# Performance work log

Measured on AMD Instinct MI355X. Metric: run time of the kernel, lower is better.

Reference implementation:

```python
import jax, jax.numpy as jnp
import numpy as np

NUM_CIRCLES = 7
B, D_IN, D_HID, D_OUT = 4096, 2048, 3584, 2048  # D_HID % 7 == 0 (7 * 512)


def setup_inputs() -> dict:
    key = jax.random.key(0)
    k1, k2, k3, k4 = jax.random.split(key, 4)
    x = jax.random.normal(k1, (B, D_IN), dtype=jnp.float32)
    # FlowerOfLife: 7 bias-free Linear(D_IN -> D_HID//7) weights, stacked [7, D_HID//7, D_IN]
    W_flower = jax.random.normal(k2, (NUM_CIRCLES, D_HID // NUM_CIRCLES, D_IN), dtype=jnp.float32) / np.sqrt(D_IN).astype(np.float32)
    # Merkaba: two bias-free Linear(D_HID -> D_OUT)
    W_male = jax.random.normal(k3, (D_OUT, D_HID), dtype=jnp.float32) / np.sqrt(D_HID).astype(np.float32)
    W_female = jax.random.normal(k4, (D_OUT, D_HID), dtype=jnp.float32) / np.sqrt(D_HID).astype(np.float32)
    return {"x": x, "W_flower": W_flower, "W_male": W_male, "W_female": W_female}


def reference(x, W_flower, W_male, W_female):
    # --- VesicaPiscisOperation: sacred overlap with the batch-rolled neighbor ---
    x2 = jnp.roll(x, 1, axis=0)
    dist = jnp.linalg.norm(x - x2, axis=1, keepdims=True)          # [B, 1]
    overlap = jax.nn.relu(1.0 - jnp.abs(dist - 1.0))               # [B, 1]
    x_overlap = x * (1.0 + overlap)                                # per-row scaling

    # --- FlowerOfLifeProjection: 7 parallel projections, phase-shift first 2 dims ---
    circ = jnp.einsum('bd,cod->bco', x_overlap, W_flower)          # [B, 7, D_HID//7]
    phases = 2.0 * jnp.pi * jnp.arange(NUM_CIRCLES, dtype=jnp.float32) / NUM_CIRCLES
    phase_shift = jnp.stack([jnp.cos(phases), jnp.sin(phases)], axis=-1)  # [7, 2]
    circ = circ.at[:, :, :2].multiply(phase_shift[None, :, :])
    x_expanded = circ.reshape(x.shape[0], -1)                      # [B, D_HID]

    # --- MerkabaRotation: counter-rotating transforms + sigmoid phase lock ---
    male = x_expanded @ W_male.T                                   # [B, D_OUT]
    female = x_expanded[:, ::-1] @ W_female.T                      # flip(-1) then Linear
    phase_lock = jax.nn.sigmoid(jnp.sum(male * female, axis=-1, keepdims=True))
    return phase_lock * male + (1.0 - phase_lock) * female
```

## Files before the change

### kernel.cpp

```cpp
#include <hip/hip_runtime.h>
#include <hip/hip_bf16.h>
#include <math.h>

#define B_DIM 4096
#define D_IN  2048
#define D_HID 3584
#define D_OUT 2048

typedef __bf16 bf16;
typedef float  floatx4 __attribute__((ext_vector_type(4)));
typedef bf16   bf16x8  __attribute__((ext_vector_type(8)));
typedef bf16   bf16x4  __attribute__((ext_vector_type(4)));

typedef __attribute__((address_space(1))) const void* gptr1;
typedef __attribute__((address_space(3))) void*       lptr3;

__device__ __forceinline__ void load_lds16(const void* g, void* l) {
    __builtin_amdgcn_global_load_lds((gptr1)g, (lptr3)l, 16, 0, 0);
}

struct HL { bf16 h, l; };
__device__ __forceinline__ HL split2(float v) {
    HL r;
    r.h = (bf16)v;
    r.l = (bf16)(v - (float)r.h);
    return r;
}

__device__ __forceinline__ void xcd_tile(int& n0, int& m0) {
    const int d  = (int)(blockIdx.x + gridDim.x * blockIdx.y);
    const int r  = d >> 3;
    const int nx = ((d & 7) << 1) | (r & 1);
    const int my = r >> 1;
    n0 = nx * 128;
    m0 = my * 128;
}

__global__ __launch_bounds__(256) void vesica_kernel(const float* __restrict__ x,
                                                     bf16* __restrict__ xh,
                                                     bf16* __restrict__ xl) {
    const int b  = blockIdx.x;
    const int bp = (b == 0) ? (B_DIM - 1) : (b - 1);
    const int t  = threadIdx.x;

    const floatx4* xr = (const floatx4*)(x + (size_t)b  * D_IN);
    const floatx4* pr = (const floatx4*)(x + (size_t)bp * D_IN);
    const floatx4 v0 = xr[t * 2], v1 = xr[t * 2 + 1];
    const floatx4 p0 = pr[t * 2], p1 = pr[t * 2 + 1];

    float s = 0.f;
#pragma unroll
    for (int j = 0; j < 4; ++j) {
        const float d0 = v0[j] - p0[j], d1 = v1[j] - p1[j];
        s += d0 * d0 + d1 * d1;
    }
#pragma unroll
    for (int off = 32; off > 0; off >>= 1) s += __shfl_down(s, off, 64);

    __shared__ float red[4];
    const int wave = t >> 6, lane = t & 63;
    if (lane == 0) red[wave] = s;
    __syncthreads();
    const float dist = sqrtf(red[0] + red[1] + red[2] + red[3]);
    const float sc   = 1.f + fmaxf(0.f, 1.f - fabsf(dist - 1.f));

    bf16x8 h, l;
#pragma unroll
    for (int j = 0; j < 4; ++j) {
        const HL a  = split2(v0[j] * sc);
        const HL b2 = split2(v1[j] * sc);
        h[j] = a.h;      l[j] = a.l;
        h[4 + j] = b2.h; l[4 + j] = b2.l;
    }
    ((bf16x8*)(xh + (size_t)b * D_IN))[t] = h;
    ((bf16x8*)(xl + (size_t)b * D_IN))[t] = l;
}

__global__ __launch_bounds__(256) void wcat_kernel(const float* __restrict__ Wm,
                                                   const float* __restrict__ Wfe,
                                                   bf16* __restrict__ wh,
                                                   bf16* __restrict__ wl) {
    const int i = blockIdx.x * 256 + threadIdx.x;
    const int o = i / 448;
    const int g = i - o * 448;
    bf16x8 h, l;
    if (o < 2048) {
        const float* src = Wm + (size_t)o * 3584 + (size_t)g * 8;
        const floatx4 a = ((const floatx4*)src)[0];
        const floatx4 b = ((const floatx4*)src)[1];
#pragma unroll
        for (int j = 0; j < 4; ++j) {
            const HL u = split2(a[j]);
            const HL v = split2(b[j]);
            h[j] = u.h;     l[j] = u.l;
            h[4 + j] = v.h; l[4 + j] = v.l;
        }
    } else {
        const float* src = Wfe + (size_t)(o - 2048) * 3584 + (size_t)(447 - g) * 8;
        const floatx4 a = ((const floatx4*)src)[0];
        const floatx4 b = ((const floatx4*)src)[1];
#pragma unroll
        for (int j = 0; j < 4; ++j) {
            const HL u = split2(b[3 - j]);
            const HL v = split2(a[3 - j]);
            h[j] = u.h;     l[j] = u.l;
            h[4 + j] = v.h; l[4 + j] = v.l;
        }
    }
    ((bf16x8*)wh)[i] = h;
    ((bf16x8*)wl)[i] = l;
}

__global__ __launch_bounds__(256) void tsplit_kernel(const float* __restrict__ w,
                                                     bf16* __restrict__ th,
                                                     bf16* __restrict__ tl) {
    __shared__ float tile[64][65];
    const int d0 = blockIdx.x * 64;
    const int h0 = blockIdx.y * 64;
    const int t  = threadIdx.x;
    const int r  = t >> 4;
    const int cg = (t & 15) << 2;

#pragma unroll
    for (int i = 0; i < 4; ++i) {
        const int hr = r + i * 16;
        const floatx4 v = *(const floatx4*)&w[(size_t)(h0 + hr) * 2048 + d0 + cg];
        tile[hr][cg]     = v[0];
        tile[hr][cg + 1] = v[1];
        tile[hr][cg + 2] = v[2];
        tile[hr][cg + 3] = v[3];
    }
    __syncthreads();

    float pm[4];
#pragma unroll
    for (int j = 0; j < 4; ++j) {
        const int h  = h0 + cg + j;
        const int hm = h & 511;
        float p = 1.f;
        if (hm < 2) {
            const float ph = 0.8975979010256552f * (float)(h >> 9);
            p = (hm == 0) ? cosf(ph) : sinf(ph);
        }
        pm[j] = p;
    }

#pragma unroll
    for (int i = 0; i < 4; ++i) {
        const int dr = r + i * 16;
        bf16x4 hh, ll;
#pragma unroll
        for (int j = 0; j < 4; ++j) {
            const HL u = split2(tile[cg + j][dr] * pm[j]);
            hh[j] = u.h;
            ll[j] = u.l;
        }
        const size_t o = (size_t)(d0 + dr) * 3584 + h0 + cg;
        *(bf16x4*)&th[o] = hh;
        *(bf16x4*)&tl[o] = ll;
    }
}

__global__ __launch_bounds__(256, 2) void gemm3_single(const bf16* __restrict__ Ah,
                                                       const bf16* __restrict__ Al,
                                                       const bf16* __restrict__ Bh,
                                                       const bf16* __restrict__ Bl,
                                                       bf16* __restrict__ C0,
                                                       bf16* __restrict__ C1,
                                                       int M, int N, int K) {
    __shared__ bf16 sAh[128 * 64], sAl[128 * 64];
    __shared__ bf16 sBh[128 * 64], sBl[128 * 64];

    const int tid  = threadIdx.x;
    const int wave = tid >> 6;
    const int lane = tid & 63;
    int n0, m0;
    xcd_tile(n0, m0);
    const int wm   = wave & 1;
    const int wn   = wave >> 1;

    floatx4 acc[4][4];
#pragma unroll
    for (int i = 0; i < 4; ++i)
#pragma unroll
        for (int j = 0; j < 4; ++j) acc[i][j] = (floatx4){0.f, 0.f, 0.f, 0.f};

    const int lr  = lane & 15;
    const int cc8 = (lane >> 4) << 3;
    const int sw  = lr & 7;

    for (int kt = 0; kt < K; kt += 64) {
#pragma unroll
        for (int i = 0; i < 4; ++i) {
            const int q = ((i * 4 + wave) << 6) + lane;
            const int r = q >> 3;
            const int c = (q & 7) ^ (r & 7);
            const int e = q << 3;
            const size_t ga = (size_t)(m0 + r) * K + kt + c * 8;
            const size_t gb = (size_t)(n0 + r) * K + kt + c * 8;
            load_lds16(&Ah[ga], &sAh[e]);
            load_lds16(&Al[ga], &sAl[e]);
            load_lds16(&Bh[gb], &sBh[e]);
            load_lds16(&Bl[gb], &sBl[e]);
        }
        __syncthreads();

#pragma unroll
        for (int ks = 0; ks < 2; ++ks) {
            const int cb = (ks << 2) + (cc8 >> 3);
            const int co = (cb ^ sw) << 3;
            bf16x8 ah[4], al[4], bh[4], bl[4];
#pragma unroll
            for (int mi = 0; mi < 4; ++mi) {
                const int off = ((wm * 64 + mi * 16 + lr) << 6) + co;
                ah[mi] = *(const bf16x8*)&sAh[off];
                al[mi] = *(const bf16x8*)&sAl[off];
            }
#pragma unroll
            for (int ni = 0; ni < 4; ++ni) {
                const int off = ((wn * 64 + ni * 16 + lr) << 6) + co;
                bh[ni] = *(const bf16x8*)&sBh[off];
                bl[ni] = *(const bf16x8*)&sBl[off];
            }

#pragma unroll
            for (int mi = 0; mi < 4; ++mi)
#pragma unroll
                for (int ni = 0; ni < 4; ++ni) {
                    acc[mi][ni] = __builtin_amdgcn_mfma_f32_16x16x32_bf16(
                        ah[mi], bh[ni], acc[mi][ni], 0, 0, 0);
                    acc[mi][ni] = __builtin_amdgcn_mfma_f32_16x16x32_bf16(
                        al[mi], bh[ni], acc[mi][ni], 0, 0, 0);
                    acc[mi][ni] = __builtin_amdgcn_mfma_f32_16x16x32_bf16(
                        ah[mi], bl[ni], acc[mi][ni], 0, 0, 0);
                }
        }
        __syncthreads();
    }

    const int rq = (lane >> 4) << 2;
    const int cl = lane & 15;
#pragma unroll
    for (int mi = 0; mi < 4; ++mi) {
#pragma unroll
        for (int ni = 0; ni < 4; ++ni) {
            const int col = n0 + wn * 64 + ni * 16 + cl;
#pragma unroll
            for (int r = 0; r < 4; ++r) {
                const int row = m0 + wm * 64 + mi * 16 + rq + r;
                const size_t idx = (size_t)row * N + col;
                const HL u = split2(acc[mi][ni][r]);
                C0[idx] = u.h;
                C1[idx] = u.l;
            }
        }
    }
}

__global__ __launch_bounds__(256, 2) void gemm3_dual(const bf16* __restrict__ Ah,
                                                     const bf16* __restrict__ Al,
                                                     const bf16* __restrict__ Bmh,
                                                     const bf16* __restrict__ Bml,
                                                     const bf16* __restrict__ Bfh,
                                                     const bf16* __restrict__ Bfl,
                                                     float* __restrict__ Cm,
                                                     float* __restrict__ Cf,
                                                     int M, int N, int K) {
    __shared__ bf16 sAh[4096], sAl[4096];
    __shared__ bf16 sMh[4096], sMl[4096];
    __shared__ bf16 sFh[4096], sFl[4096];

    const int tid  = threadIdx.x;
    const int wave = tid >> 6;
    const int lane = tid & 63;
    int n0, m0;
    xcd_tile(n0, m0);
    const int wm   = wave & 1;
    const int wn   = wave >> 1;

    floatx4 am[4][4], af[4][4];
#pragma unroll
    for (int i = 0; i < 4; ++i)
#pragma unroll
        for (int j = 0; j < 4; ++j) {
            am[i][j] = (floatx4){0.f, 0.f, 0.f, 0.f};
            af[i][j] = (floatx4){0.f, 0.f, 0.f, 0.f};
        }

    const int lr  = lane & 15;
    const int cc8 = (lane >> 4) << 3;
    const int cq  = cc8 >> 3;
    const int hsw = lr >> 1;

    for (int kt = 0; kt < K; kt += 32) {
#pragma unroll
        for (int i = 0; i < 2; ++i) {
            const int q = ((i * 4 + wave) << 6) + lane;
            const int p = q ^ ((q >> 3) & 7);
            const int r = p >> 2, c = p & 3;
            const int e = q << 3;
            const size_t ga = (size_t)(m0 + r) * K + kt + c * 8;
            const size_t gb = (size_t)(n0 + r) * K + kt + c * 8;
            load_lds16(&Ah[ga],  &sAh[e]);
            load_lds16(&Al[ga],  &sAl[e]);
            load_lds16(&Bmh[gb], &sMh[e]);
            load_lds16(&Bml[gb], &sMl[e]);
            load_lds16(&Bfh[gb], &sFh[e]);
            load_lds16(&Bfl[gb], &sFl[e]);
        }
        __syncthreads();

        bf16x8 ah[4], al[4];
#pragma unroll
        for (int mi = 0; mi < 4; ++mi) {
            const int ql  = ((wm * 64 + mi * 16 + lr) << 2) + cq;
            const int off = (ql ^ hsw) << 3;
            ah[mi] = *(const bf16x8*)&sAh[off];
            al[mi] = *(const bf16x8*)&sAl[off];
        }
#pragma unroll
        for (int ni = 0; ni < 4; ++ni) {
            const int ql  = ((wn * 64 + ni * 16 + lr) << 2) + cq;
            const int off = (ql ^ hsw) << 3;
            const bf16x8 mh = *(const bf16x8*)&sMh[off];
            const bf16x8 ml = *(const bf16x8*)&sMl[off];
            const bf16x8 fh = *(const bf16x8*)&sFh[off];
            const bf16x8 fl = *(const bf16x8*)&sFl[off];
#pragma unroll
            for (int mi = 0; mi < 4; ++mi) {
                am[mi][ni] = __builtin_amdgcn_mfma_f32_16x16x32_bf16(
                    ah[mi], mh, am[mi][ni], 0, 0, 0);
                am[mi][ni] = __builtin_amdgcn_mfma_f32_16x16x32_bf16(
                    al[mi], mh, am[mi][ni], 0, 0, 0);
                am[mi][ni] = __builtin_amdgcn_mfma_f32_16x16x32_bf16(
                    ah[mi], ml, am[mi][ni], 0, 0, 0);
                af[mi][ni] = __builtin_amdgcn_mfma_f32_16x16x32_bf16(
                    ah[mi], fh, af[mi][ni], 0, 0, 0);
                af[mi][ni] = __builtin_amdgcn_mfma_f32_16x16x32_bf16(
                    al[mi], fh, af[mi][ni], 0, 0, 0);
                af[mi][ni] = __builtin_amdgcn_mfma_f32_16x16x32_bf16(
                    ah[mi], fl, af[mi][ni], 0, 0, 0);
            }
        }
        __syncthreads();
    }

    const int rq = (lane >> 4) << 2;
    const int cl = lane & 15;
#pragma unroll
    for (int mi = 0; mi < 4; ++mi) {
#pragma unroll
        for (int ni = 0; ni < 4; ++ni) {
            const int col = n0 + wn * 64 + ni * 16 + cl;
#pragma unroll
            for (int r = 0; r < 4; ++r) {
                const int row = m0 + wm * 64 + mi * 16 + rq + r;
                const size_t idx = (size_t)row * N + col;
                Cm[idx] = am[mi][ni][r];
                Cf[idx] = af[mi][ni][r];
            }
        }
    }
}

__global__ __launch_bounds__(256) void combine_kernel(const float* __restrict__ male,
                                                      const float* __restrict__ female,
                                                      float* __restrict__ out) {
    const int b = blockIdx.x;
    const int t = threadIdx.x;

    const floatx4* m4 = (const floatx4*)(male   + (size_t)b * D_OUT);
    const floatx4* f4 = (const floatx4*)(female + (size_t)b * D_OUT);
    const floatx4 mv0 = m4[t * 2], mv1 = m4[t * 2 + 1];
    const floatx4 fv0 = f4[t * 2], fv1 = f4[t * 2 + 1];

    float s = 0.f;
#pragma unroll
    for (int j = 0; j < 4; ++j) s += mv0[j] * fv0[j] + mv1[j] * fv1[j];
#pragma unroll
    for (int off = 32; off > 0; off >>= 1) s += __shfl_down(s, off, 64);

    __shared__ float red[4];
    const int wave = t >> 6, lane = t & 63;
    if (lane == 0) red[wave] = s;
    __syncthreads();
    const float dot = red[0] + red[1] + red[2] + red[3];
    const float pl  = 1.f / (1.f + expf(-dot));

    floatx4 o0, o1;
#pragma unroll
    for (int j = 0; j < 4; ++j) {
        o0[j] = pl * mv0[j] + (1.f - pl) * fv0[j];
        o1[j] = pl * mv1[j] + (1.f - pl) * fv1[j];
    }
    floatx4* o4 = (floatx4*)(out + (size_t)b * D_OUT);
    o4[t * 2]     = o0;
    o4[t * 2 + 1] = o1;
}

extern "C" void kernel_launch(void* const* d_in, const int* in_sizes, int n_in,
                              void* d_out, int out_size, void* d_ws, size_t ws_size,
                              hipStream_t stream) {
    const float* x   = (const float*)d_in[0];
    const float* Wfl = (const float*)d_in[1];
    const float* Wm  = (const float*)d_in[2];
    const float* Wfe = (const float*)d_in[3];
    float* out = (float*)d_out;
    (void)in_sizes; (void)n_in; (void)out_size; (void)ws_size;

    char* ws = (char*)d_ws;
    bf16*  xo_hi   = (bf16*)(ws);
    bf16*  xo_lo   = (bf16*)(ws + 16777216);
    bf16*  Wc_hi   = (bf16*)(ws + 33554432);
    bf16*  Wc_lo   = (bf16*)(ws + 50331648);
    bf16*  WflT_hi = (bf16*)(ws + 67108864);
    bf16*  WflT_lo = (bf16*)(ws + 81788928);
    bf16*  Wcat_hi = (bf16*)(ws + 96468992);
    bf16*  Wcat_lo = (bf16*)(ws + 125829120);
    float* male    = (float*)(ws + 67108864);
    float* female  = (float*)(ws + 100663296);

    vesica_kernel<<<B_DIM, 256, 0, stream>>>(x, xo_hi, xo_lo);

    tsplit_kernel<<<dim3(D_IN / 64, D_HID / 64), 256, 0, stream>>>(Wfl, WflT_hi, WflT_lo);

    wcat_kernel<<<(2 * D_OUT * (D_HID / 8)) / 256, 256, 0, stream>>>(
        Wm, Wfe, Wcat_hi, Wcat_lo);

    gemm3_single<<<dim3(D_IN / 128, (2 * D_OUT) / 128), 256, 0, stream>>>(
        Wcat_hi, Wcat_lo, WflT_hi, WflT_lo, Wc_hi, Wc_lo,
        2 * D_OUT, D_IN, D_HID);

    gemm3_dual<<<dim3(D_OUT / 128, B_DIM / 128), 256, 0, stream>>>(
        xo_hi, xo_lo,
        Wc_hi, Wc_lo,
        Wc_hi + (size_t)D_OUT * D_IN, Wc_lo + (size_t)D_OUT * D_IN,
        male, female, B_DIM, D_OUT, D_IN);

    combine_kernel<<<B_DIM, 256, 0, stream>>>(male, female, out);
}
```

Measured before the change: 476.8 us.

## Switch GEMMs to 32x32x16 MFMA and merge the three prep kernels into one launch

After: 515.0 us. 1.08x slower.

```diff
diff --git a/kernel.cpp b/kernel.cpp
--- a/kernel.cpp
+++ b/kernel.cpp
@@ -8,9 +8,10 @@
 #define D_OUT 2048
 
 typedef __bf16 bf16;
-typedef float  floatx4 __attribute__((ext_vector_type(4)));
-typedef bf16   bf16x8  __attribute__((ext_vector_type(8)));
-typedef bf16   bf16x4  __attribute__((ext_vector_type(4)));
+typedef float  floatx4  __attribute__((ext_vector_type(4)));
+typedef float  floatx16 __attribute__((ext_vector_type(16)));
+typedef bf16   bf16x8   __attribute__((ext_vector_type(8)));
+typedef bf16   bf16x4   __attribute__((ext_vector_type(4)));
 
 typedef __attribute__((address_space(1))) const void* gptr1;
 typedef __attribute__((address_space(3))) void*       lptr3;
@@ -36,128 +37,132 @@
     m0 = my * 128;
 }
 
-__global__ __launch_bounds__(256) void vesica_kernel(const float* __restrict__ x,
-                                                     bf16* __restrict__ xh,
-                                                     bf16* __restrict__ xl) {
-    const int b  = blockIdx.x;
-    const int bp = (b == 0) ? (B_DIM - 1) : (b - 1);
-    const int t  = threadIdx.x;
-
-    const floatx4* xr = (const floatx4*)(x + (size_t)b  * D_IN);
-    const floatx4* pr = (const floatx4*)(x + (size_t)bp * D_IN);
-    const floatx4 v0 = xr[t * 2], v1 = xr[t * 2 + 1];
-    const floatx4 p0 = pr[t * 2], p1 = pr[t * 2 + 1];
-
-    float s = 0.f;
-#pragma unroll
-    for (int j = 0; j < 4; ++j) {
-        const float d0 = v0[j] - p0[j], d1 = v1[j] - p1[j];
-        s += d0 * d0 + d1 * d1;
-    }
-#pragma unroll
-    for (int off = 32; off > 0; off >>= 1) s += __shfl_down(s, off, 64);
-
-    __shared__ float red[4];
-    const int wave = t >> 6, lane = t & 63;
-    if (lane == 0) red[wave] = s;
-    __syncthreads();
-    const float dist = sqrtf(red[0] + red[1] + red[2] + red[3]);
-    const float sc   = 1.f + fmaxf(0.f, 1.f - fabsf(dist - 1.f));
-
-    bf16x8 h, l;
-#pragma unroll
-    for (int j = 0; j < 4; ++j) {
-        const HL a  = split2(v0[j] * sc);
-        const HL b2 = split2(v1[j] * sc);
-        h[j] = a.h;      l[j] = a.l;
-        h[4 + j] = b2.h; l[4 + j] = b2.l;
-    }
-    ((bf16x8*)(xh + (size_t)b * D_IN))[t] = h;
-    ((bf16x8*)(xl + (size_t)b * D_IN))[t] = l;
-}
-
-__global__ __launch_bounds__(256) void wcat_kernel(const float* __restrict__ Wm,
+__global__ __launch_bounds__(256) void prep_kernel(const float* __restrict__ x,
+                                                   const float* __restrict__ Wfl,
+                                                   const float* __restrict__ Wm,
                                                    const float* __restrict__ Wfe,
+                                                   bf16* __restrict__ xh,
+                                                   bf16* __restrict__ xl,
+                                                   bf16* __restrict__ th,
+                                                   bf16* __restrict__ tl,
                                                    bf16* __restrict__ wh,
                                                    bf16* __restrict__ wl) {
-    const int i = blockIdx.x * 256 + threadIdx.x;
-    const int o = i / 448;
-    const int g = i - o * 448;
-    bf16x8 h, l;
-    if (o < 2048) {
-        const float* src = Wm + (size_t)o * 3584 + (size_t)g * 8;
-        const floatx4 a = ((const floatx4*)src)[0];
-        const floatx4 b = ((const floatx4*)src)[1];
+    __shared__ float tile[64][65];
+    const int id = blockIdx.x;
+    const int t  = threadIdx.x;
+
+    if (id < 4096) {
+        const int b  = id;
+        const int bp = (b == 0) ? (B_DIM - 1) : (b - 1);
+
+        const floatx4* xr = (const floatx4*)(x + (size_t)b  * D_IN);
+        const floatx4* pr = (const floatx4*)(x + (size_t)bp * D_IN);
+        const floatx4 v0 = xr[t * 2], v1 = xr[t * 2 + 1];
+        const floatx4 p0 = pr[t * 2], p1 = pr[t * 2 + 1];
+
+        float s = 0.f;
 #pragma unroll
         for (int j = 0; j < 4; ++j) {
-            const HL u = split2(a[j]);
-            const HL v = split2(b[j]);
-            h[j] = u.h;     l[j] = u.l;
-            h[4 + j] = v.h; l[4 + j] = v.l;
-        }
+            const float d0 = v0[j] - p0[j], d1 = v1[j] - p1[j];
+            s += d0 * d0 + d1 * d1;
+        }
+#pragma unroll
+        for (int off = 32; off > 0; off >>= 1) s += __shfl_down(s, off, 64);
+
+        float* red = &tile[0][0];
+        const int wave = t >> 6, lane = t & 63;
+        if (lane == 0) red[wave] = s;
+        __syncthreads();
+        const float dist = sqrtf(red[0] + red[1] + red[2] + red[3]);
+        const float sc   = 1.f + fmaxf(0.f, 1.f - fabsf(dist - 1.f));
+
+        bf16x8 h, l;
+#pragma unroll
+        for (int j = 0; j < 4; ++j) {
+            const HL a  = split2(v0[j] * sc);
+            const HL b2 = split2(v1[j] * sc);
+            h[j] = a.h;      l[j] = a.l;
+            h[4 + j] = b2.h; l[4 + j] = b2.l;
+        }
+        ((bf16x8*)(xh + (size_t)b * D_IN))[t] = h;
+        ((bf16x8*)(xl + (size_t)b * D_IN))[t] = l;
+
+    } else if (id < 4096 + 1792) {
+        const int tb = id - 4096;
+        const int d0 = (tb & 31) << 6;
+        const int h0 = (tb >> 5) << 6;
+        const int r  = t >> 4;
+        const int cg = (t & 15) << 2;
+
+#pragma unroll
+        for (int i = 0; i < 4; ++i) {
+            const int hr = r + i * 16;
+            const floatx4 v = *(const floatx4*)&Wfl[(size_t)(h0 + hr) * 2048 + d0 + cg];
+            tile[hr][cg]     = v[0];
+            tile[hr][cg + 1] = v[1];
+            tile[hr][cg + 2] = v[2];
+            tile[hr][cg + 3] = v[3];
+        }
+        __syncthreads();
+
+        float pm[4];
+#pragma unroll
+        for (int j = 0; j < 4; ++j) {
+            const int h  = h0 + cg + j;
+            const int hm = h & 511;
+            float p = 1.f;
+            if (hm < 2) {
+                const float ph = 0.8975979010256552f * (float)(h >> 9);
+                p = (hm == 0) ? cosf(ph) : sinf(ph);
+            }
+            pm[j] = p;
+        }
+
+#pragma unroll
+        for (int i = 0; i < 4; ++i) {
+            const int dr = r + i * 16;
+            bf16x4 hh, ll;
+#pragma unroll
+            for (int j = 0; j < 4; ++j) {
+                const HL u = split2(tile[cg + j][dr] * pm[j]);
+                hh[j] = u.h;
+                ll[j] = u.l;
+            }
+            const size_t o = (size_t)(d0 + dr) * 3584 + h0 + cg;
+            *(bf16x4*)&th[o] = hh;
+            *(bf16x4*)&tl[o] = ll;
+        }
+
     } else {
-        const float* src = Wfe + (size_t)(o - 2048) * 3584 + (size_t)(447 - g) * 8;
-        const floatx4 a = ((const floatx4*)src)[0];
-        const floatx4 b = ((const floatx4*)src)[1];
-#pragma unroll
-        for (int j = 0; j < 4; ++j) {
-            const HL u = split2(b[3 - j]);
-            const HL v = split2(a[3 - j]);
-            h[j] = u.h;     l[j] = u.l;
-            h[4 + j] = v.h; l[4 + j] = v.l;
-        }
-    }
-    ((bf16x8*)wh)[i] = h;
-    ((bf16x8*)wl)[i] = l;
-}
-
-__global__ __launch_bounds__(256) void tsplit_kernel(const float* __restrict__ w,
-                                                     bf16* __restrict__ th,
-                                                     bf16* __restrict__ tl) {
-    __shared__ float tile[64][65];
-    const int d0 = blockIdx.x * 64;
-    const int h0 = blockIdx.y * 64;
-    const int t  = threadIdx.x;
-    const int r  = t >> 4;
-    const int cg = (t & 15) << 2;
-
-#pragma unroll
-    for (int i = 0; i < 4; ++i) {
-        const int hr = r + i * 16;
-        const floatx4 v = *(const floatx4*)&w[(size_t)(h0 + hr) * 2048 + d0 + cg];
-        tile[hr][cg]     = v[0];
-        tile[hr][cg + 1] = v[1];
-        tile[hr][cg + 2] = v[2];
-        tile[hr][cg + 3] = v[3];
-    }
-    __syncthreads();
-
-    float pm[4];
-#pragma unroll
-    for (int j = 0; j < 4; ++j) {
-        const int h  = h0 + cg + j;
-        const int hm = h & 511;
-        float p = 1.f;
-        if (hm < 2) {
-            const float ph = 0.8975979010256552f * (float)(h >> 9);
-            p = (hm == 0) ? cosf(ph) : sinf(ph);
-        }
-        pm[j] = p;
-    }
-
-#pragma unroll
-    for (int i = 0; i < 4; ++i) {
-        const int dr = r + i * 16;
-        bf16x4 hh, ll;
-#pragma unroll
-        for (int j = 0; j < 4; ++j) {
-            const HL u = split2(tile[cg + j][dr] * pm[j]);
-            hh[j] = u.h;
-            ll[j] = u.l;
-        }
-        const size_t o = (size_t)(d0 + dr) * 3584 + h0 + cg;
-        *(bf16x4*)&th[o] = hh;
-        *(bf16x4*)&tl[o] = ll;
+        const int i = (id - 5888) * 256 + t;
+        const int o = i / 448;
+        const int g = i - o * 448;
+        bf16x8 h, l;
+        if (o < 2048) {
+            const float* src = Wm + (size_t)o * 3584 + (size_t)g * 8;
+            const floatx4 a = ((const floatx4*)src)[0];
+            const floatx4 b = ((const floatx4*)src)[1];
+#pragma unroll
+            for (int j = 0; j < 4; ++j) {
+                const HL u = split2(a[j]);
+                const HL v = split2(b[j]);
+                h[j] = u.h;     l[j] = u.l;
+                h[4 + j] = v.h; l[4 + j] = v.l;
+            }
+        } else {
+            const float* src = Wfe + (size_t)(o - 2048) * 3584 + (size_t)(447 - g) * 8;
+            const floatx4 a = ((const floatx4*)src)[0];
+            const floatx4 b = ((const floatx4*)src)[1];
+#pragma unroll
+            for (int j = 0; j < 4; ++j) {
+                const HL u = split2(b[3 - j]);
+                const HL v = split2(a[3 - j]);
+                h[j] = u.h;     l[j] = u.l;
+                h[4 + j] = v.h; l[4 + j] = v.l;
+            }
+        }
+        ((bf16x8*)wh)[i] = h;
+        ((bf16x8*)wl)[i] = l;
     }
 }
 
@@ -179,15 +184,17 @@
     const int wm   = wave & 1;
     const int wn   = wave >> 1;
 
-    floatx4 acc[4][4];
-#pragma unroll
-    for (int i = 0; i < 4; ++i)
-#pragma unroll
-        for (int j = 0; j < 4; ++j) acc[i][j] = (floatx4){0.f, 0.f, 0.f, 0.f};
-
-    const int lr  = lane & 15;
-    const int cc8 = (lane >> 4) << 3;
-    const int sw  = lr & 7;
+    const floatx16 fz = {0.f,0.f,0.f,0.f,0.f,0.f,0.f,0.f,
+                         0.f,0.f,0.f,0.f,0.f,0.f,0.f,0.f};
+    floatx16 acc[2][2];
+#pragma unroll
+    for (int i = 0; i < 2; ++i)
+#pragma unroll
+        for (int j = 0; j < 2; ++j) acc[i][j] = fz;
+
+    const int l31 = lane & 31;
+    const int kh  = lane >> 5;
+    const int sw7 = l31 & 7;
 
     for (int kt = 0; kt < K; kt += 64) {
 #pragma unroll
@@ -206,55 +213,54 @@
         __syncthreads();
 
 #pragma unroll
-        for (int ks = 0; ks < 2; ++ks) {
-            const int cb = (ks << 2) + (cc8 >> 3);
-            const int co = (cb ^ sw) << 3;
-            bf16x8 ah[4], al[4], bh[4], bl[4];
-#pragma unroll
-            for (int mi = 0; mi < 4; ++mi) {
-                const int off = ((wm * 64 + mi * 16 + lr) << 6) + co;
-                ah[mi] = *(const bf16x8*)&sAh[off];
-                al[mi] = *(const bf16x8*)&sAl[off];
-            }
-#pragma unroll
-            for (int ni = 0; ni < 4; ++ni) {
-                const int off = ((wn * 64 + ni * 16 + lr) << 6) + co;
-                bh[ni] = *(const bf16x8*)&sBh[off];
-                bl[ni] = *(const bf16x8*)&sBl[off];
-            }
-
-#pragma unroll
-            for (int mi = 0; mi < 4; ++mi)
-#pragma unroll
-                for (int ni = 0; ni < 4; ++ni) {
-                    acc[mi][ni] = __builtin_amdgcn_mfma_f32_16x16x32_bf16(
-                        ah[mi], bh[ni], acc[mi][ni], 0, 0, 0);
-                    acc[mi][ni] = __builtin_amdgcn_mfma_f32_16x16x32_bf16(
-                        al[mi], bh[ni], acc[mi][ni], 0, 0, 0);
-                    acc[mi][ni] = __builtin_amdgcn_mfma_f32_16x16x32_bf16(
-                        ah[mi], bl[ni], acc[mi][ni], 0, 0, 0);
+        for (int ks = 0; ks < 4; ++ks) {
+            const int cb = (ks << 1) + kh;
+            bf16x8 ah[2], al[2], bh[2], bl[2];
+#pragma unroll
+            for (int mb = 0; mb < 2; ++mb) {
+                const int row = wm * 64 + mb * 32 + l31;
+                const int off = ((row << 3) | (cb ^ sw7)) << 3;
+                ah[mb] = *(const bf16x8*)&sAh[off];
+                al[mb] = *(const bf16x8*)&sAl[off];
+            }
+#pragma unroll
+            for (int nb = 0; nb < 2; ++nb) {
+                const int row = wn * 64 + nb * 32 + l31;
+                const int off = ((row << 3) | (cb ^ sw7)) << 3;
+                bh[nb] = *(const bf16x8*)&sBh[off];
+                bl[nb] = *(const bf16x8*)&sBl[off];
+            }
+
+#pragma unroll
+            for (int mb = 0; mb < 2; ++mb)
+#pragma unroll
+                for (int nb = 0; nb < 2; ++nb) {
+                    acc[mb][nb] = __builtin_amdgcn_mfma_f32_32x32x16_bf16(
+                        ah[mb], bh[nb], acc[mb][nb], 0, 0, 0);
+                    acc[mb][nb] = __builtin_amdgcn_mfma_f32_32x32x16_bf16(
+                        al[mb], bh[nb], acc[mb][nb], 0, 0, 0);
+                    acc[mb][nb] = __builtin_amdgcn_mfma_f32_32x32x16_bf16(
+                        ah[mb], bl[nb], acc[mb][nb], 0, 0, 0);
                 }
         }
         __syncthreads();
     }
 
-    const int rq = (lane >> 4) << 2;
-    const int cl = lane & 15;
-#pragma unroll
-    for (int mi = 0; mi < 4; ++mi) {
-#pragma unroll
-        for (int ni = 0; ni < 4; ++ni) {
-            const int col = n0 + wn * 64 + ni * 16 + cl;
-#pragma unroll
-            for (int r = 0; r < 4; ++r) {
-                const int row = m0 + wm * 64 + mi * 16 + rq + r;
+#pragma unroll
+    for (int mb = 0; mb < 2; ++mb)
+#pragma unroll
+        for (int nb = 0; nb < 2; ++nb) {
+            const int col = n0 + wn * 64 + nb * 32 + l31;
+#pragma unroll
+            for (int reg = 0; reg < 16; ++reg) {
+                const int row = m0 + wm * 64 + mb * 32 +
+                                (reg & 3) + ((reg >> 2) << 3) + (kh << 2);
                 const size_t idx = (size_t)row * N + col;
-                const HL u = split2(acc[mi][ni][r]);
+                const HL u = split2(acc[mb][nb][reg]);
                 C0[idx] = u.h;
                 C1[idx] = u.l;
             }
         }
-    }
 }
 
 __global__ __launch_bounds__(256, 2) void gemm3_dual(const bf16* __restrict__ Ah,
@@ -278,19 +284,17 @@
     const int wm   = wave & 1;
     const int wn   = wave >> 1;
 
-    floatx4 am[4][4], af[4][4];
-#pragma unroll
-    for (int i = 0; i < 4; ++i)
-#pragma unroll
-        for (int j = 0; j < 4; ++j) {
-            am[i][j] = (floatx4){0.f, 0.f, 0.f, 0.f};
-            af[i][j] = (floatx4){0.f, 0.f, 0.f, 0.f};
-        }
-
-    const int lr  = lane & 15;
-    const int cc8 = (lane >> 4) << 3;
-    const int cq  = cc8 >> 3;
-    const int hsw = lr >> 1;
+    const floatx16 fz = {0.f,0.f,0.f,0.f,0.f,0.f,0.f,0.f,
+                         0.f,0.f,0.f,0.f,0.f,0.f,0.f,0.f};
+    floatx16 am[2][2], af[2][2];
+#pragma unroll
+    for (int i = 0; i < 2; ++i)
+#pragma unroll
+        for (int j = 0; j < 2; ++j) { am[i][j] = fz; af[i][j] = fz; }
+
+    const int l31 = lane & 31;
+    const int kh  = lane >> 5;
+    const int rsw = (l31 >> 1) & 7;
 
     for (int kt = 0; kt < K; kt += 32) {
 #pragma unroll
@@ -310,57 +314,59 @@
         }
         __syncthreads();
 
-        bf16x8 ah[4], al[4];
-#pragma unroll
-        for (int mi = 0; mi < 4; ++mi) {
-            const int ql  = ((wm * 64 + mi * 16 + lr) << 2) + cq;
-            const int off = (ql ^ hsw) << 3;
-            ah[mi] = *(const bf16x8*)&sAh[off];
-            al[mi] = *(const bf16x8*)&sAl[off];
-        }
-#pragma unroll
-        for (int ni = 0; ni < 4; ++ni) {
-            const int ql  = ((wn * 64 + ni * 16 + lr) << 2) + cq;
-            const int off = (ql ^ hsw) << 3;
-            const bf16x8 mh = *(const bf16x8*)&sMh[off];
-            const bf16x8 ml = *(const bf16x8*)&sMl[off];
-            const bf16x8 fh = *(const bf16x8*)&sFh[off];
-            const bf16x8 fl = *(const bf16x8*)&sFl[off];
-#pragma unroll
-            for (int mi = 0; mi < 4; ++mi) {
-                am[mi][ni] = __builtin_amdgcn_mfma_f32_16x16x32_bf16(
-                    ah[mi], mh, am[mi][ni], 0, 0, 0);
-                am[mi][ni] = __builtin_amdgcn_mfma_f32_16x16x32_bf16(
-                    al[mi], mh, am[mi][ni], 0, 0, 0);
-                am[mi][ni] = __builtin_amdgcn_mfma_f32_16x16x32_bf16(
-                    ah[mi], ml, am[mi][ni], 0, 0, 0);
-                af[mi][ni] = __builtin_amdgcn_mfma_f32_16x16x32_bf16(
-                    ah[mi], fh, af[mi][ni], 0, 0, 0);
-                af[mi][ni] = __builtin_amdgcn_mfma_f32_16x16x32_bf16(
-                    al[mi], fh, af[mi][ni], 0, 0, 0);
-                af[mi][ni] = __builtin_amdgcn_mfma_f32_16x16x32_bf16(
-                    ah[mi], fl, af[mi][ni], 0, 0, 0);
+#pragma unroll
+        for (int kk = 0; kk < 2; ++kk) {
+            const int cb = (kk << 1) + kh;
+            bf16x8 ah[2], al[2];
+#pragma unroll
+            for (int mb = 0; mb < 2; ++mb) {
+                const int row = wm * 64 + mb * 32 + l31;
+                const int off = ((((row << 2) + cb) ^ rsw)) << 3;
+                ah[mb] = *(const bf16x8*)&sAh[off];
+                al[mb] = *(const bf16x8*)&sAl[off];
+            }
+#pragma unroll
+            for (int nb = 0; nb < 2; ++nb) {
+                const int row = wn * 64 + nb * 32 + l31;
+                const int off = ((((row << 2) + cb) ^ rsw)) << 3;
+                const bf16x8 mh = *(const bf16x8*)&sMh[off];
+                const bf16x8 ml = *(const bf16x8*)&sMl[off];
+                const bf16x8 fh = *(const bf16x8*)&sFh[off];
+                const bf16x8 fl = *(const bf16x8*)&sFl[off];
+#pragma unroll
+                for (int mb = 0; mb < 2; ++mb) {
+                    am[mb][nb] = __builtin_amdgcn_mfma_f32_32x32x16_bf16(
+                        ah[mb], mh, am[mb][nb], 0, 0, 0);
+                    am[mb][nb] = __builtin_amdgcn_mfma_f32_32x32x16_bf16(
+                        al[mb], mh, am[mb][nb], 0, 0, 0);
+                    am[mb][nb] = __builtin_amdgcn_mfma_f32_32x32x16_bf16(
+                        ah[mb], ml, am[mb][nb], 0, 0, 0);
+                    af[mb][nb] = __builtin_amdgcn_mfma_f32_32x32x16_bf16(
+                        ah[mb], fh, af[mb][nb], 0, 0, 0);
+                    af[mb][nb] = __builtin_amdgcn_mfma_f32_32x32x16_bf16(
+                        al[mb], fh, af[mb][nb], 0, 0, 0);
+                    af[mb][nb] = __builtin_amdgcn_mfma_f32_32x32x16_bf16(
+                        ah[mb], fl, af[mb][nb], 0, 0, 0);
+                }
             }
         }
         __syncthreads();
     }
 
-    const int rq = (lane >> 4) << 2;
-    const int cl = lane & 15;
-#pragma unroll
-    for (int mi = 0; mi < 4; ++mi) {
-#pragma unroll
-        for (int ni = 0; ni < 4; ++ni) {
-            const int col = n0 + wn * 64 + ni * 16 + cl;
-#pragma unroll
-            for (int r = 0; r < 4; ++r) {
-                const int row = m0 + wm * 64 + mi * 16 + rq + r;
+#pragma unroll
+    for (int mb = 0; mb < 2; ++mb)
+#pragma unroll
+        for (int nb = 0; nb < 2; ++nb) {
+            const int col = n0 + wn * 64 + nb * 32 + l31;
+#pragma unroll
+            for (int reg = 0; reg < 16; ++reg) {
+                const int row = m0 + wm * 64 + mb * 32 +
+                                (reg & 3) + ((reg >> 2) << 3) + (kh << 2);
                 const size_t idx = (size_t)row * N + col;
-                Cm[idx] = am[mi][ni][r];
-                Cf[idx] = af[mi][ni][r];
-            }
-        }
-    }
+                Cm[idx] = am[mb][nb][reg];
+                Cf[idx] = af[mb][nb][reg];
+            }
+        }
 }
 
 __global__ __launch_bounds__(256) void combine_kernel(const float* __restrict__ male,
@@ -420,12 +426,10 @@
     float* male    = (float*)(ws + 67108864);
     float* female  = (float*)(ws + 100663296);
 
-    vesica_kernel<<<B_DIM, 256, 0, stream>>>(x, xo_hi, xo_lo);
-
-    tsplit_kernel<<<dim3(D_IN / 64, D_HID / 64), 256, 0, stream>>>(Wfl, WflT_hi, WflT_lo);
-
-    wcat_kernel<<<(2 * D_OUT * (D_HID / 8)) / 256, 256, 0, stream>>>(
-        Wm, Wfe, Wcat_hi, Wcat_lo);
+    prep_kernel<<<13056, 256, 0, stream>>>(x, Wfl, Wm, Wfe,
+                                           xo_hi, xo_lo,
+                                           WflT_hi, WflT_lo,
+                                           Wcat_hi, Wcat_lo);
 
     gemm3_single<<<dim3(D_IN / 128, (2 * D_OUT) / 128), 256, 0, stream>>>(
         Wcat_hi, Wcat_lo, WflT_hi, WflT_lo, Wc_hi, Wc_lo,
```
